# Kernel tuning notes

Measured on AMD Instinct MI355X. Metric: run time of the kernel, lower is better.

The kernel has to match this reference:

```python
import jax, jax.numpy as jnp
import numpy as np

N_NODES = 200000
FEAT_DIM = 256
EMB_DIM = 64
N_EXP = 100000
N_TARGETS = 1024
MAX_CAND = 128


def setup_inputs() -> dict:
    key = jax.random.key(0)
    ks = jax.random.split(key, 10)
    return {
        "x": jax.random.normal(ks[0], (N_NODES, FEAT_DIM), jnp.float32),
        "h": jax.random.normal(ks[1], (N_NODES, EMB_DIM), jnp.float32),
        "degree": jax.random.uniform(ks[2], (N_NODES,), jnp.float32),
        "beta": jax.random.uniform(ks[3], (N_NODES,), jnp.float32),
        "exp_nodes": jax.random.randint(ks[4], (N_EXP,), 0, N_NODES),
        "idx_targets": jax.random.randint(ks[5], (N_TARGETS,), 0, N_NODES),
        "W_raw": jax.random.normal(ks[6], (FEAT_DIM, EMB_DIM), jnp.float32) / np.float32(np.sqrt(FEAT_DIM)),
        "b_raw": jnp.zeros((EMB_DIM,), jnp.float32),
        "W_num": jax.random.normal(ks[7], (2, EMB_DIM), jnp.float32),
        "b_num": jnp.zeros((EMB_DIM,), jnp.float32),
        "W1": jax.random.normal(ks[8], (4 * EMB_DIM, EMB_DIM), jnp.float32) / np.float32(np.sqrt(4 * EMB_DIM)),
        "b1": jnp.zeros((EMB_DIM,), jnp.float32),
        "W2": jax.random.normal(ks[9], (EMB_DIM, 1), jnp.float32) / np.float32(np.sqrt(EMB_DIM)),
        "b2": jnp.zeros((1,), jnp.float32),
        "temperature": jnp.float32(1.0),
        "epsilon": jnp.float32(1.0),
    }


def reference(x, h, degree, beta, exp_nodes, idx_targets,
              W_raw, b_raw, W_num, b_num, W1, b1, W2, b2,
              temperature, epsilon):
    # gather node features and project (irregular gather + small GEMM)
    x_v = x[exp_nodes] @ W_raw + b_raw                       # [E, emb]
    h_v = h[exp_nodes]                                       # [E, emb]
    h_T = jnp.broadcast_to(h[idx_targets].mean(axis=0)[None, :],
                           (exp_nodes.shape[0], EMB_DIM))    # [E, emb]
    numerics = jnp.stack([degree[exp_nodes], beta[exp_nodes]], axis=-1)  # [E, 2]
    emb_num = numerics @ W_num + b_num                       # [E, emb]
    emb = jax.nn.relu(jnp.concatenate([x_v, h_v, h_T, emb_num], axis=-1))  # [E, 4*emb]
    # dropout is identity in eval mode
    hidden = jax.nn.relu(emb @ W1 + b1)                      # [E, emb]
    scores = (hidden @ W2 + b2)[:, 0]                        # [E]
    # straight-through gumbel top-k (eval: no gumbel noise, epsilon unused)
    y = jax.nn.softmax(scores / temperature)
    _, idx = jax.lax.top_k(y, MAX_CAND)
    y_hard = jnp.zeros_like(y).at[idx].set(1.0)
    y_st = jax.lax.stop_gradient(y_hard - y) + y
    candidates = y_st[idx]                                   # [MAX_CAND] (== 1.0 fwd)
    cand_indices = exp_nodes[idx]                            # [MAX_CAND]
    return candidates, cand_indices
```

## Files before the change

### kernel.cpp

```cpp
#include <hip/hip_runtime.h>
#include <stdint.h>

#define RELU(v) ((v) > 0.0f ? (v) : 0.0f)

typedef unsigned long long u64;
typedef unsigned int u32;
typedef unsigned short u16;
typedef float f32x4 __attribute__((ext_vector_type(4)));
typedef short bf16x8 __attribute__((ext_vector_type(8)));

constexpr int FEAT = 256;
constexpr int EMB  = 64;

constexpr int STG_ROW = 264;
constexpr int WAVE_BYTES = 16 * STG_ROW * 2;
constexpr int XV_ROW = 68;
constexpr int KEEP_BLK = 12;

__device__ inline u16 bf16_trunc(float v) { return (u16)(__float_as_uint(v) >> 16); }

__device__ inline u32 score_key(float s) {
    u32 u = __float_as_uint(s);
    return (u & 0x80000000u) ? ~u : (u | 0x80000000u);
}

__device__ inline bf16x8 pack_bf16x8(float4 lo, float4 hi) {
    bf16x8 r;
    r[0] = (short)bf16_trunc(lo.x); r[1] = (short)bf16_trunc(lo.y);
    r[2] = (short)bf16_trunc(lo.z); r[3] = (short)bf16_trunc(lo.w);
    r[4] = (short)bf16_trunc(hi.x); r[5] = (short)bf16_trunc(hi.y);
    r[6] = (short)bf16_trunc(hi.z); r[7] = (short)bf16_trunc(hi.w);
    return r;
}

__global__ __launch_bounds__(1024) void setup_kernel(
    const float* __restrict__ h, const int* __restrict__ idx_targets, int nT,
    const float* __restrict__ W_raw, const float* __restrict__ W1, const float* __restrict__ b1,
    float* __restrict__ bias_eff, u16* __restrict__ wrawpk, u16* __restrict__ w1pk)
{
    const int tid = threadIdx.x;
    if (blockIdx.x == 1) {
        for (int t = tid; t < 2048; t += 1024) {
            int ks   = t >> 8;
            int c    = (t >> 6) & 3;
            int lane = t & 63;
            int n    = c * 16 + (lane & 15);
            int kbase = ks * 32 + ((lane >> 4) << 3);
            #pragma unroll
            for (int j = 0; j < 8; ++j) {
                int k = kbase + j;
                wrawpk[t * 8 + j] = bf16_trunc(W_raw[(size_t)k * EMB + n]);
                w1pk  [t * 8 + j] = bf16_trunc(W1   [(size_t)k * EMB + n]);
            }
        }
        return;
    }
    __shared__ int   idx_s[1024];
    __shared__ float partial[16][64];
    __shared__ float hT[64];
    const int nid = nT > 1024 ? 1024 : nT;
    for (int i = tid; i < nid; i += 1024) idx_s[i] = idx_targets[i];
    __syncthreads();
    const int d = tid & 63, grp = tid >> 6;
    float s = 0.f;
    for (int t = grp; t < nid; t += 16)
        s += h[(size_t)idx_s[t] * EMB + d];
    partial[grp][d] = s;
    __syncthreads();
    if (tid < 64) {
        float m = 0.f;
        #pragma unroll
        for (int g = 0; g < 16; ++g) m += partial[g][tid];
        hT[tid] = RELU(m / (float)nT);
    }
    __syncthreads();
    if (tid < 64) {
        float acc = b1[tid];
        #pragma unroll 8
        for (int dd = 0; dd < 64; ++dd)
            acc = fmaf(hT[dd], W1[(size_t)(128 + dd) * EMB + tid], acc);
        bias_eff[tid] = acc;
    }
}

__global__ __launch_bounds__(256) void approx_score_kernel(
    const float* __restrict__ x, const float* __restrict__ h,
    const float* __restrict__ degree, const float* __restrict__ beta,
    const int* __restrict__ exp_nodes,
    const u16* __restrict__ wrawpk, const u16* __restrict__ w1pk,
    const float* __restrict__ b_raw,
    const float* __restrict__ W_num, const float* __restrict__ b_num,
    const float* __restrict__ W2, const float* __restrict__ bias_eff,
    u64* __restrict__ cand1, int E)
{
    __shared__ __align__(16) unsigned char smem[4][WAVE_BYTES];
    __shared__ u64 sarr[64];

    const int tid  = threadIdx.x;
    const int wid  = tid >> 6;
    const int lane = tid & 63;
    const int rloc = lane & 15;
    const int kgrp = lane >> 4;
    const int koff = kgrp * 8;
    const int tileBase = blockIdx.x * 64;

    const int grow = tileBase + wid * 16 + rloc;
    const int node = exp_nodes[grow < E ? grow : 0];
    const float* hrow = h + (size_t)node * EMB;
    const float dg = degree[node];
    const float bt = beta[node];

    u16*   stg = (u16*)&smem[wid][0];
    float* xvp = (float*)&smem[wid][0];

    #pragma unroll
    for (int half = 0; half < 2; ++half) {
        float4 v0, v1, v2, v3, v4, v5, v6, v7;
        {
            int r = half * 8;
            v0 = *reinterpret_cast<const float4*>(x + (size_t)__shfl(node, r + 0) * FEAT + lane * 4);
            v1 = *reinterpret_cast<const float4*>(x + (size_t)__shfl(node, r + 1) * FEAT + lane * 4);
            v2 = *reinterpret_cast<const float4*>(x + (size_t)__shfl(node, r + 2) * FEAT + lane * 4);
            v3 = *reinterpret_cast<const float4*>(x + (size_t)__shfl(node, r + 3) * FEAT + lane * 4);
            v4 = *reinterpret_cast<const float4*>(x + (size_t)__shfl(node, r + 4) * FEAT + lane * 4);
            v5 = *reinterpret_cast<const float4*>(x + (size_t)__shfl(node, r + 5) * FEAT + lane * 4);
            v6 = *reinterpret_cast<const float4*>(x + (size_t)__shfl(node, r + 6) * FEAT + lane * 4);
            v7 = *reinterpret_cast<const float4*>(x + (size_t)__shfl(node, r + 7) * FEAT + lane * 4);
        }
        #define STG_WRITE(rr, vv) { \
            ushort4 pk; pk.x = bf16_trunc(vv.x); pk.y = bf16_trunc(vv.y); \
            pk.z = bf16_trunc(vv.z); pk.w = bf16_trunc(vv.w); \
            *reinterpret_cast<ushort4*>(stg + (half * 8 + rr) * STG_ROW + lane * 4) = pk; }
        STG_WRITE(0, v0) STG_WRITE(1, v1) STG_WRITE(2, v2) STG_WRITE(3, v3)
        STG_WRITE(4, v4) STG_WRITE(5, v5) STG_WRITE(6, v6) STG_WRITE(7, v7)
        #undef STG_WRITE
    }
    __builtin_amdgcn_wave_barrier();

    f32x4 acc1[4];
    #pragma unroll
    for (int c = 0; c < 4; ++c) {
        float bv = b_raw[c * 16 + rloc];
        acc1[c] = (f32x4){bv, bv, bv, bv};
    }
    #pragma unroll
    for (int ks = 0; ks < 8; ++ks) {
        bf16x8 a = *reinterpret_cast<const bf16x8*>(stg + rloc * STG_ROW + ks * 32 + koff);
        #pragma unroll
        for (int c = 0; c < 4; ++c) {
            bf16x8 b = *reinterpret_cast<const bf16x8*>(wrawpk + (size_t)((ks * 4 + c) * 64 + lane) * 8);
            acc1[c] = __builtin_amdgcn_mfma_f32_16x16x32_bf16(a, b, acc1[c], 0, 0, 0);
        }
    }
    __builtin_amdgcn_wave_barrier();

    #pragma unroll
    for (int c = 0; c < 4; ++c)
        #pragma unroll
        for (int r = 0; r < 4; ++r)
            xvp[(kgrp * 4 + r) * XV_ROW + c * 16 + rloc] = RELU(acc1[c][r]);
    __builtin_amdgcn_wave_barrier();

    f32x4 acc2[4];
    #pragma unroll
    for (int c = 0; c < 4; ++c) {
        float bv = bias_eff[c * 16 + rloc];
        acc2[c] = (f32x4){bv, bv, bv, bv};
    }

    #pragma unroll
    for (int ks = 0; ks < 2; ++ks) {
        float4 lo = *reinterpret_cast<const float4*>(hrow + ks * 32 + koff);
        float4 hi = *reinterpret_cast<const float4*>(hrow + ks * 32 + koff + 4);
        lo.x = RELU(lo.x); lo.y = RELU(lo.y); lo.z = RELU(lo.z); lo.w = RELU(lo.w);
        hi.x = RELU(hi.x); hi.y = RELU(hi.y); hi.z = RELU(hi.z); hi.w = RELU(hi.w);
        bf16x8 a = pack_bf16x8(lo, hi);
        #pragma unroll
        for (int c = 0; c < 4; ++c) {
            bf16x8 b = *reinterpret_cast<const bf16x8*>(w1pk + (size_t)(((2 + ks) * 4 + c) * 64 + lane) * 8);
            acc2[c] = __builtin_amdgcn_mfma_f32_16x16x32_bf16(a, b, acc2[c], 0, 0, 0);
        }
    }

    #pragma unroll
    for (int ks = 0; ks < 2; ++ks) {
        bf16x8 a;
        #pragma unroll
        for (int j = 0; j < 8; ++j) {
            int k = ks * 32 + koff + j;
            float v = RELU(fmaf(dg, W_num[k], fmaf(bt, W_num[EMB + k], b_num[k])));
            a[j] = (short)bf16_trunc(v);
        }
        #pragma unroll
        for (int c = 0; c < 4; ++c) {
            bf16x8 b = *reinterpret_cast<const bf16x8*>(w1pk + (size_t)(((6 + ks) * 4 + c) * 64 + lane) * 8);
            acc2[c] = __builtin_amdgcn_mfma_f32_16x16x32_bf16(a, b, acc2[c], 0, 0, 0);
        }
    }

    #pragma unroll
    for (int ks = 0; ks < 2; ++ks) {
        float4 lo = *reinterpret_cast<const float4*>(xvp + rloc * XV_ROW + ks * 32 + koff);
        float4 hi = *reinterpret_cast<const float4*>(xvp + rloc * XV_ROW + ks * 32 + koff + 4);
        bf16x8 a = pack_bf16x8(lo, hi);
        #pragma unroll
        for (int c = 0; c < 4; ++c) {
            bf16x8 b = *reinterpret_cast<const bf16x8*>(w1pk + (size_t)((ks * 4 + c) * 64 + lane) * 8);
            acc2[c] = __builtin_amdgcn_mfma_f32_16x16x32_bf16(a, b, acc2[c], 0, 0, 0);
        }
    }

    float p[4] = {0.f, 0.f, 0.f, 0.f};
    #pragma unroll
    for (int c = 0; c < 4; ++c) {
        float w2v = W2[c * 16 + rloc];
        #pragma unroll
        for (int r = 0; r < 4; ++r)
            p[r] = fmaf(RELU(acc2[c][r]), w2v, p[r]);
    }
    #pragma unroll
    for (int m = 1; m < 16; m <<= 1) {
        p[0] += __shfl_xor(p[0], m);
        p[1] += __shfl_xor(p[1], m);
        p[2] += __shfl_xor(p[2], m);
        p[3] += __shfl_xor(p[3], m);
    }
    if (rloc == 0) {
        #pragma unroll
        for (int r = 0; r < 4; ++r) {
            int lrow = wid * 16 + kgrp * 4 + r;
            int g = tileBase + lrow;
            sarr[lrow] = (g < E) ? (((u64)score_key(p[r]) << 32) | (u32)(~(u32)g)) : 0ULL;
        }
    }
    __syncthreads();

    if (wid == 0) {
        u64 v = sarr[lane];
        #pragma unroll
        for (int k = 2; k <= 64; k <<= 1) {
            #pragma unroll
            for (int j = k >> 1; j > 0; j >>= 1) {
                u64 o = __shfl_xor(v, j);
                bool lower = (lane & j) == 0;
                bool dir   = (lane & k) == 0;
                v = (lower == dir) ? (v > o ? v : o) : (v < o ? v : o);
            }
        }
        if (lane < KEEP_BLK) cand1[(size_t)blockIdx.x * KEEP_BLK + lane] = v;
    }
}

template<int N, int NT>
__device__ inline void bitonic_desc(u64* s, int tid) {
    for (int k = 2; k <= N; k <<= 1) {
        for (int j = k >> 1; j > 0; j >>= 1) {
            __syncthreads();
            for (int i = tid; i < N; i += NT) {
                int ixj = i ^ j;
                if (ixj > i) {
                    u64 a = s[i], b = s[ixj];
                    bool sw = ((i & k) == 0) ? (a < b) : (a > b);
                    if (sw) { s[i] = b; s[ixj] = a; }
                }
            }
        }
    }
    __syncthreads();
}

template<int N, int NT, int KEEP>
__global__ __launch_bounds__(NT) void seg_sort_kernel(
    const u64* __restrict__ in, int n_in, int seg, u64* __restrict__ out)
{
    __shared__ u64 s[N];
    int tid = threadIdx.x;
    int base = blockIdx.x * seg;
    for (int i = tid; i < N; i += NT) {
        int g = base + i;
        s[i] = (i < seg && g < n_in) ? in[g] : 0ULL;
    }
    bitonic_desc<N, NT>(s, tid);
    if (tid < KEEP) out[blockIdx.x * KEEP + tid] = s[tid];
}

__global__ __launch_bounds__(256) void rescore_kernel(
    const float* __restrict__ x, const float* __restrict__ h,
    const float* __restrict__ degree, const float* __restrict__ beta,
    const int* __restrict__ exp_nodes,
    const float* __restrict__ W_raw, const float* __restrict__ b_raw,
    const float* __restrict__ W_num, const float* __restrict__ b_num,
    const float* __restrict__ W1, const float* __restrict__ W2,
    const float* __restrict__ bias_eff,
    const u64* __restrict__ cand, u64* __restrict__ pairs2, int E)
{
    __shared__ float emb[4][192];
    const int tid = threadIdx.x;
    const int wid = tid >> 6;
    const int c   = tid & 63;
    const int i   = blockIdx.x * 4 + wid;

    const u64 raw = cand[i];
    const u32 low = (u32)raw;
    const u32 ge  = ~low;
    const int node = (raw != 0ULL && ge < (u32)E) ? exp_nodes[ge] : 0;

    const float* xrow = x + (size_t)node * FEAT;

    float s0 = b_raw[c], s1 = 0.f, s2 = 0.f, s3 = 0.f;
    for (int k = 0; k < FEAT; k += 4) {
        s0 = fmaf(xrow[k + 0], W_raw[(size_t)(k + 0) * EMB + c], s0);
        s1 = fmaf(xrow[k + 1], W_raw[(size_t)(k + 1) * EMB + c], s1);
        s2 = fmaf(xrow[k + 2], W_raw[(size_t)(k + 2) * EMB + c], s2);
        s3 = fmaf(xrow[k + 3], W_raw[(size_t)(k + 3) * EMB + c], s3);
    }
    float xv = (s0 + s1) + (s2 + s3);

    emb[wid][c]       = RELU(xv);
    emb[wid][64 + c]  = RELU(h[(size_t)node * EMB + c]);
    emb[wid][128 + c] = RELU(fmaf(degree[node], W_num[c], fmaf(beta[node], W_num[EMB + c], b_num[c])));
    __syncthreads();

    float h0 = bias_eff[c], h1 = 0.f, h2 = 0.f, h3 = 0.f;
    for (int j = 0; j < 64; j += 2) {
        h0 = fmaf(emb[wid][j],     W1[(size_t)j * EMB + c],       h0);
        h1 = fmaf(emb[wid][j + 1], W1[(size_t)(j + 1) * EMB + c], h1);
    }
    for (int j = 0; j < 64; j += 2) {
        h2 = fmaf(emb[wid][64 + j],     W1[(size_t)(64 + j) * EMB + c],     h2);
        h3 = fmaf(emb[wid][64 + j + 1], W1[(size_t)(64 + j + 1) * EMB + c], h3);
    }
    for (int j = 0; j < 64; j += 2) {
        h0 = fmaf(emb[wid][128 + j],     W1[(size_t)(192 + j) * EMB + c],     h0);
        h1 = fmaf(emb[wid][128 + j + 1], W1[(size_t)(192 + j + 1) * EMB + c], h1);
    }
    float hid = (h0 + h1) + (h2 + h3);

    float p = RELU(hid) * W2[c];
    #pragma unroll
    for (int m = 1; m < 64; m <<= 1) p += __shfl_xor(p, m);

    if (c == 0)
        pairs2[i] = (raw == 0ULL) ? 0ULL : (((u64)score_key(p) << 32) | low);
}

__global__ __launch_bounds__(1024) void topk_final_kernel(
    const u64* __restrict__ in, int n_in,
    const int* __restrict__ exp_nodes, float* __restrict__ out)
{
    __shared__ u64 s[1024];
    int tid = threadIdx.x;
    s[tid] = (tid < n_in) ? in[tid] : 0ULL;
    bitonic_desc<1024, 1024>(s, tid);
    if (tid < 128) {
        u64 p = s[tid];
        u32 idx = ~(u32)(p & 0xFFFFFFFFu);
        out[tid]       = 1.0f;
        out[128 + tid] = (float)exp_nodes[idx];
    }
}

extern "C" void kernel_launch(void* const* d_in, const int* in_sizes, int n_in,
                              void* d_out, int out_size, void* d_ws, size_t ws_size,
                              hipStream_t stream) {
    const float* x          = (const float*)d_in[0];
    const float* h          = (const float*)d_in[1];
    const float* degree     = (const float*)d_in[2];
    const float* beta       = (const float*)d_in[3];
    const int*   exp_nodes  = (const int*)d_in[4];
    const int*   idx_targets= (const int*)d_in[5];
    const float* W_raw      = (const float*)d_in[6];
    const float* b_raw      = (const float*)d_in[7];
    const float* W_num      = (const float*)d_in[8];
    const float* b_num      = (const float*)d_in[9];
    const float* W1         = (const float*)d_in[10];
    const float* b1         = (const float*)d_in[11];
    const float* W2         = (const float*)d_in[12];

    int E  = in_sizes[4];
    int nT = in_sizes[5];

    int nTiles = (E + 63) / 64;
    int nCand1 = nTiles * KEEP_BLK;
    int nSel   = (nCand1 + 1023) / 1024;
    int nKept  = nSel * 52;
    int nResc  = (nKept + 3) / 4;

    char* ws = (char*)d_ws;
    float* bias_eff = (float*)ws;
    u16* wrawpk = (u16*)(ws + 256);
    u16* w1pk   = (u16*)(ws + 256 + 32768);
    u64* cand1  = (u64*)(ws + 256 + 65536);
    u64* cand2  = (u64*)(ws + 256 + 65536 + 163840);
    u64* pairs2 = (u64*)(ws + 256 + 65536 + 163840 + 8192);

    setup_kernel<<<2, 1024, 0, stream>>>(h, idx_targets, nT, W_raw, W1, b1,
                                         bias_eff, wrawpk, w1pk);

    approx_score_kernel<<<nTiles, 256, 0, stream>>>(x, h, degree, beta, exp_nodes,
                                                    wrawpk, w1pk, b_raw, W_num, b_num,
                                                    W2, bias_eff, cand1, E);

    seg_sort_kernel<1024, 512, 52><<<nSel, 512, 0, stream>>>(cand1, nCand1, 1024, cand2);

    rescore_kernel<<<nResc, 256, 0, stream>>>(x, h, degree, beta, exp_nodes,
                                              W_raw, b_raw, W_num, b_num, W1, W2,
                                              bias_eff, cand2, pairs2, E);

    topk_final_kernel<<<1, 1024, 0, stream>>>(pairs2, nKept, exp_nodes, (float*)d_out);
}
```

Measured before the change: 107.8 us.

## Double rows per wave in approx scoring, fuse final top-k into rescore

The approx score kernel now handles 128 rows per block, 32 per wave. Each wave loads x rows straight from global into MFMA A-fragments instead of staging bf16 copies in LDS, and two accumulator sets share each loaded weight fragment. The final top-k kernel is folded into the rescore kernel: an atomic counter picks the last-finishing block, which does the bitonic sort, and a memset resets the counter on every call. This cuts one launch and the LDS staging traffic, but raises register pressure and loads x with narrower per-lane strided accesses.

```diff
diff --git a/kernel.cpp b/kernel.cpp
--- a/kernel.cpp
+++ b/kernel.cpp
@@ -12,8 +12,6 @@
 constexpr int FEAT = 256;
 constexpr int EMB  = 64;
 
-constexpr int STG_ROW = 264;
-constexpr int WAVE_BYTES = 16 * STG_ROW * 2;
 constexpr int XV_ROW = 68;
 constexpr int KEEP_BLK = 12;
 
@@ -93,8 +91,8 @@
     const float* __restrict__ W2, const float* __restrict__ bias_eff,
     u64* __restrict__ cand1, int E)
 {
-    __shared__ __align__(16) unsigned char smem[4][WAVE_BYTES];
-    __shared__ u64 sarr[64];
+    __shared__ __align__(16) float xv_lds[4][32 * XV_ROW];
+    __shared__ u64 sarr[128];
 
     const int tid  = threadIdx.x;
     const int wid  = tid >> 6;
@@ -102,141 +100,149 @@
     const int rloc = lane & 15;
     const int kgrp = lane >> 4;
     const int koff = kgrp * 8;
-    const int tileBase = blockIdx.x * 64;
-
-    const int grow = tileBase + wid * 16 + rloc;
-    const int node = exp_nodes[grow < E ? grow : 0];
-    const float* hrow = h + (size_t)node * EMB;
-    const float dg = degree[node];
-    const float bt = beta[node];
-
-    u16*   stg = (u16*)&smem[wid][0];
-    float* xvp = (float*)&smem[wid][0];
-
-    #pragma unroll
-    for (int half = 0; half < 2; ++half) {
-        float4 v0, v1, v2, v3, v4, v5, v6, v7;
-        {
-            int r = half * 8;
-            v0 = *reinterpret_cast<const float4*>(x + (size_t)__shfl(node, r + 0) * FEAT + lane * 4);
-            v1 = *reinterpret_cast<const float4*>(x + (size_t)__shfl(node, r + 1) * FEAT + lane * 4);
-            v2 = *reinterpret_cast<const float4*>(x + (size_t)__shfl(node, r + 2) * FEAT + lane * 4);
-            v3 = *reinterpret_cast<const float4*>(x + (size_t)__shfl(node, r + 3) * FEAT + lane * 4);
-            v4 = *reinterpret_cast<const float4*>(x + (size_t)__shfl(node, r + 4) * FEAT + lane * 4);
-            v5 = *reinterpret_cast<const float4*>(x + (size_t)__shfl(node, r + 5) * FEAT + lane * 4);
-            v6 = *reinterpret_cast<const float4*>(x + (size_t)__shfl(node, r + 6) * FEAT + lane * 4);
-            v7 = *reinterpret_cast<const float4*>(x + (size_t)__shfl(node, r + 7) * FEAT + lane * 4);
-        }
-        #define STG_WRITE(rr, vv) { \
-            ushort4 pk; pk.x = bf16_trunc(vv.x); pk.y = bf16_trunc(vv.y); \
-            pk.z = bf16_trunc(vv.z); pk.w = bf16_trunc(vv.w); \
-            *reinterpret_cast<ushort4*>(stg + (half * 8 + rr) * STG_ROW + lane * 4) = pk; }
-        STG_WRITE(0, v0) STG_WRITE(1, v1) STG_WRITE(2, v2) STG_WRITE(3, v3)
-        STG_WRITE(4, v4) STG_WRITE(5, v5) STG_WRITE(6, v6) STG_WRITE(7, v7)
-        #undef STG_WRITE
-    }
-    __builtin_amdgcn_wave_barrier();
-
-    f32x4 acc1[4];
+    const int tileBase = blockIdx.x * 128;
+
+    const int g0 = tileBase + wid * 32 + rloc;
+    const int g1 = g0 + 16;
+    const int node0 = exp_nodes[g0 < E ? g0 : 0];
+    const int node1 = exp_nodes[g1 < E ? g1 : 0];
+    const float* xrow0 = x + (size_t)node0 * FEAT;
+    const float* xrow1 = x + (size_t)node1 * FEAT;
+    const float* hrow0 = h + (size_t)node0 * EMB;
+    const float* hrow1 = h + (size_t)node1 * EMB;
+    const float dg0 = degree[node0], bt0 = beta[node0];
+    const float dg1 = degree[node1], bt1 = beta[node1];
+
+    float* xvpA = &xv_lds[wid][0];
+    float* xvpB = &xv_lds[wid][16 * XV_ROW];
+
+    f32x4 acc1a[4], acc1b[4];
     #pragma unroll
     for (int c = 0; c < 4; ++c) {
         float bv = b_raw[c * 16 + rloc];
-        acc1[c] = (f32x4){bv, bv, bv, bv};
+        acc1a[c] = (f32x4){bv, bv, bv, bv};
+        acc1b[c] = (f32x4){bv, bv, bv, bv};
     }
     #pragma unroll
     for (int ks = 0; ks < 8; ++ks) {
-        bf16x8 a = *reinterpret_cast<const bf16x8*>(stg + rloc * STG_ROW + ks * 32 + koff);
+        float4 lo0 = *reinterpret_cast<const float4*>(xrow0 + ks * 32 + koff);
+        float4 hi0 = *reinterpret_cast<const float4*>(xrow0 + ks * 32 + koff + 4);
+        float4 lo1 = *reinterpret_cast<const float4*>(xrow1 + ks * 32 + koff);
+        float4 hi1 = *reinterpret_cast<const float4*>(xrow1 + ks * 32 + koff + 4);
+        bf16x8 a0 = pack_bf16x8(lo0, hi0);
+        bf16x8 a1 = pack_bf16x8(lo1, hi1);
         #pragma unroll
         for (int c = 0; c < 4; ++c) {
             bf16x8 b = *reinterpret_cast<const bf16x8*>(wrawpk + (size_t)((ks * 4 + c) * 64 + lane) * 8);
-            acc1[c] = __builtin_amdgcn_mfma_f32_16x16x32_bf16(a, b, acc1[c], 0, 0, 0);
-        }
-    }
+            acc1a[c] = __builtin_amdgcn_mfma_f32_16x16x32_bf16(a0, b, acc1a[c], 0, 0, 0);
+            acc1b[c] = __builtin_amdgcn_mfma_f32_16x16x32_bf16(a1, b, acc1b[c], 0, 0, 0);
+        }
+    }
+
+    #pragma unroll
+    for (int c = 0; c < 4; ++c)
+        #pragma unroll
+        for (int r = 0; r < 4; ++r) {
+            xvpA[(kgrp * 4 + r) * XV_ROW + c * 16 + rloc] = RELU(acc1a[c][r]);
+            xvpB[(kgrp * 4 + r) * XV_ROW + c * 16 + rloc] = RELU(acc1b[c][r]);
+        }
     __builtin_amdgcn_wave_barrier();
 
-    #pragma unroll
-    for (int c = 0; c < 4; ++c)
-        #pragma unroll
-        for (int r = 0; r < 4; ++r)
-            xvp[(kgrp * 4 + r) * XV_ROW + c * 16 + rloc] = RELU(acc1[c][r]);
-    __builtin_amdgcn_wave_barrier();
-
-    f32x4 acc2[4];
+    f32x4 acc2a[4], acc2b[4];
     #pragma unroll
     for (int c = 0; c < 4; ++c) {
         float bv = bias_eff[c * 16 + rloc];
-        acc2[c] = (f32x4){bv, bv, bv, bv};
+        acc2a[c] = (f32x4){bv, bv, bv, bv};
+        acc2b[c] = (f32x4){bv, bv, bv, bv};
     }
 
     #pragma unroll
     for (int ks = 0; ks < 2; ++ks) {
-        float4 lo = *reinterpret_cast<const float4*>(hrow + ks * 32 + koff);
-        float4 hi = *reinterpret_cast<const float4*>(hrow + ks * 32 + koff + 4);
-        lo.x = RELU(lo.x); lo.y = RELU(lo.y); lo.z = RELU(lo.z); lo.w = RELU(lo.w);
-        hi.x = RELU(hi.x); hi.y = RELU(hi.y); hi.z = RELU(hi.z); hi.w = RELU(hi.w);
-        bf16x8 a = pack_bf16x8(lo, hi);
+        float4 lo0 = *reinterpret_cast<const float4*>(hrow0 + ks * 32 + koff);
+        float4 hi0 = *reinterpret_cast<const float4*>(hrow0 + ks * 32 + koff + 4);
+        float4 lo1 = *reinterpret_cast<const float4*>(hrow1 + ks * 32 + koff);
+        float4 hi1 = *reinterpret_cast<const float4*>(hrow1 + ks * 32 + koff + 4);
+        lo0.x=RELU(lo0.x); lo0.y=RELU(lo0.y); lo0.z=RELU(lo0.z); lo0.w=RELU(lo0.w);
+        hi0.x=RELU(hi0.x); hi0.y=RELU(hi0.y); hi0.z=RELU(hi0.z); hi0.w=RELU(hi0.w);
+        lo1.x=RELU(lo1.x); lo1.y=RELU(lo1.y); lo1.z=RELU(lo1.z); lo1.w=RELU(lo1.w);
+        hi1.x=RELU(hi1.x); hi1.y=RELU(hi1.y); hi1.z=RELU(hi1.z); hi1.w=RELU(hi1.w);
+        bf16x8 a0 = pack_bf16x8(lo0, hi0);
+        bf16x8 a1 = pack_bf16x8(lo1, hi1);
         #pragma unroll
         for (int c = 0; c < 4; ++c) {
             bf16x8 b = *reinterpret_cast<const bf16x8*>(w1pk + (size_t)(((2 + ks) * 4 + c) * 64 + lane) * 8);
-            acc2[c] = __builtin_amdgcn_mfma_f32_16x16x32_bf16(a, b, acc2[c], 0, 0, 0);
+            acc2a[c] = __builtin_amdgcn_mfma_f32_16x16x32_bf16(a0, b, acc2a[c], 0, 0, 0);
+            acc2b[c] = __builtin_amdgcn_mfma_f32_16x16x32_bf16(a1, b, acc2b[c], 0, 0, 0);
         }
     }
 
     #pragma unroll
     for (int ks = 0; ks < 2; ++ks) {
-        bf16x8 a;
+        bf16x8 a0, a1;
         #pragma unroll
         for (int j = 0; j < 8; ++j) {
             int k = ks * 32 + koff + j;
-            float v = RELU(fmaf(dg, W_num[k], fmaf(bt, W_num[EMB + k], b_num[k])));
-            a[j] = (short)bf16_trunc(v);
+            float wn0 = W_num[k], wn1 = W_num[EMB + k], bn = b_num[k];
+            a0[j] = (short)bf16_trunc(RELU(fmaf(dg0, wn0, fmaf(bt0, wn1, bn))));
+            a1[j] = (short)bf16_trunc(RELU(fmaf(dg1, wn0, fmaf(bt1, wn1, bn))));
         }
         #pragma unroll
         for (int c = 0; c < 4; ++c) {
             bf16x8 b = *reinterpret_cast<const bf16x8*>(w1pk + (size_t)(((6 + ks) * 4 + c) * 64 + lane) * 8);
-            acc2[c] = __builtin_amdgcn_mfma_f32_16x16x32_bf16(a, b, acc2[c], 0, 0, 0);
+            acc2a[c] = __builtin_amdgcn_mfma_f32_16x16x32_bf16(a0, b, acc2a[c], 0, 0, 0);
+            acc2b[c] = __builtin_amdgcn_mfma_f32_16x16x32_bf16(a1, b, acc2b[c], 0, 0, 0);
         }
     }
 
     #pragma unroll
     for (int ks = 0; ks < 2; ++ks) {
-        float4 lo = *reinterpret_cast<const float4*>(xvp + rloc * XV_ROW + ks * 32 + koff);
-        float4 hi = *reinterpret_cast<const float4*>(xvp + rloc * XV_ROW + ks * 32 + koff + 4);
-        bf16x8 a = pack_bf16x8(lo, hi);
+        float4 lo0 = *reinterpret_cast<const float4*>(xvpA + rloc * XV_ROW + ks * 32 + koff);
+        float4 hi0 = *reinterpret_cast<const float4*>(xvpA + rloc * XV_ROW + ks * 32 + koff + 4);
+        float4 lo1 = *reinterpret_cast<const float4*>(xvpB + rloc * XV_ROW + ks * 32 + koff);
+        float4 hi1 = *reinterpret_cast<const float4*>(xvpB + rloc * XV_ROW + ks * 32 + koff + 4);
+        bf16x8 a0 = pack_bf16x8(lo0, hi0);
+        bf16x8 a1 = pack_bf16x8(lo1, hi1);
         #pragma unroll
         for (int c = 0; c < 4; ++c) {
             bf16x8 b = *reinterpret_cast<const bf16x8*>(w1pk + (size_t)((ks * 4 + c) * 64 + lane) * 8);
-            acc2[c] = __builtin_amdgcn_mfma_f32_16x16x32_bf16(a, b, acc2[c], 0, 0, 0);
-        }
-    }
-
-    float p[4] = {0.f, 0.f, 0.f, 0.f};
+            acc2a[c] = __builtin_amdgcn_mfma_f32_16x16x32_bf16(a0, b, acc2a[c], 0, 0, 0);
+            acc2b[c] = __builtin_amdgcn_mfma_f32_16x16x32_bf16(a1, b, acc2b[c], 0, 0, 0);
+        }
+    }
+
+    float pA[4] = {0,0,0,0}, pB[4] = {0,0,0,0};
     #pragma unroll
     for (int c = 0; c < 4; ++c) {
         float w2v = W2[c * 16 + rloc];
         #pragma unroll
-        for (int r = 0; r < 4; ++r)
-            p[r] = fmaf(RELU(acc2[c][r]), w2v, p[r]);
+        for (int r = 0; r < 4; ++r) {
+            pA[r] = fmaf(RELU(acc2a[c][r]), w2v, pA[r]);
+            pB[r] = fmaf(RELU(acc2b[c][r]), w2v, pB[r]);
+        }
     }
     #pragma unroll
     for (int m = 1; m < 16; m <<= 1) {
-        p[0] += __shfl_xor(p[0], m);
-        p[1] += __shfl_xor(p[1], m);
-        p[2] += __shfl_xor(p[2], m);
-        p[3] += __shfl_xor(p[3], m);
+        #pragma unroll
+        for (int r = 0; r < 4; ++r) {
+            pA[r] += __shfl_xor(pA[r], m);
+            pB[r] += __shfl_xor(pB[r], m);
+        }
     }
     if (rloc == 0) {
         #pragma unroll
         for (int r = 0; r < 4; ++r) {
-            int lrow = wid * 16 + kgrp * 4 + r;
-            int g = tileBase + lrow;
-            sarr[lrow] = (g < E) ? (((u64)score_key(p[r]) << 32) | (u32)(~(u32)g)) : 0ULL;
-        }
-    }
-    __syncthreads();
-
-    if (wid == 0) {
-        u64 v = sarr[lane];
+            int lrowA = wid * 32 + kgrp * 4 + r;
+            int gA = tileBase + lrowA;
+            sarr[lrowA] = (gA < E) ? (((u64)score_key(pA[r]) << 32) | (u32)(~(u32)gA)) : 0ULL;
+            int lrowB = lrowA + 16;
+            int gB = tileBase + lrowB;
+            sarr[lrowB] = (gB < E) ? (((u64)score_key(pB[r]) << 32) | (u32)(~(u32)gB)) : 0ULL;
+        }
+    }
+    __syncthreads();
+
+    if (wid < 2) {
+        u64 v = sarr[wid * 64 + lane];
         #pragma unroll
         for (int k = 2; k <= 64; k <<= 1) {
             #pragma unroll
@@ -247,7 +253,8 @@
                 v = (lower == dir) ? (v > o ? v : o) : (v < o ? v : o);
             }
         }
-        if (lane < KEEP_BLK) cand1[(size_t)blockIdx.x * KEEP_BLK + lane] = v;
+        if (lane < KEEP_BLK)
+            cand1[(size_t)blockIdx.x * (2 * KEEP_BLK) + wid * KEEP_BLK + lane] = v;
     }
 }
 
@@ -284,7 +291,7 @@
     if (tid < KEEP) out[blockIdx.x * KEEP + tid] = s[tid];
 }
 
-__global__ __launch_bounds__(256) void rescore_kernel(
+__global__ __launch_bounds__(256) void rescore_final_kernel(
     const float* __restrict__ x, const float* __restrict__ h,
     const float* __restrict__ degree, const float* __restrict__ beta,
     const int* __restrict__ exp_nodes,
@@ -292,9 +299,13 @@
     const float* __restrict__ W_num, const float* __restrict__ b_num,
     const float* __restrict__ W1, const float* __restrict__ W2,
     const float* __restrict__ bias_eff,
-    const u64* __restrict__ cand, u64* __restrict__ pairs2, int E)
+    const u64* __restrict__ cand, u64* __restrict__ pairs2, int E,
+    int nKept, int nBlocks, u32* __restrict__ counter,
+    float* __restrict__ out)
 {
     __shared__ float emb[4][192];
+    __shared__ u64 s[1024];
+    __shared__ int isLast;
     const int tid = threadIdx.x;
     const int wid = tid >> 6;
     const int c   = tid & 63;
@@ -342,19 +353,22 @@
 
     if (c == 0)
         pairs2[i] = (raw == 0ULL) ? 0ULL : (((u64)score_key(p) << 32) | low);
-}
-
-__global__ __launch_bounds__(1024) void topk_final_kernel(
-    const u64* __restrict__ in, int n_in,
-    const int* __restrict__ exp_nodes, float* __restrict__ out)
-{
-    __shared__ u64 s[1024];
-    int tid = threadIdx.x;
-    s[tid] = (tid < n_in) ? in[tid] : 0ULL;
-    bitonic_desc<1024, 1024>(s, tid);
+
+    __threadfence();
+    if (tid == 0) {
+        u32 old = atomicAdd(counter, 1u);
+        isLast = (old == (u32)(nBlocks - 1));
+    }
+    __syncthreads();
+    if (!isLast) return;
+    __threadfence();
+
+    for (int k = tid; k < 1024; k += 256)
+        s[k] = (k < nKept) ? pairs2[k] : 0ULL;
+    bitonic_desc<1024, 256>(s, tid);
     if (tid < 128) {
-        u64 p = s[tid];
-        u32 idx = ~(u32)(p & 0xFFFFFFFFu);
+        u64 pr = s[tid];
+        u32 idx = ~(u32)(pr & 0xFFFFFFFFu);
         out[tid]       = 1.0f;
         out[128 + tid] = (float)exp_nodes[idx];
     }
@@ -380,8 +394,8 @@
     int E  = in_sizes[4];
     int nT = in_sizes[5];
 
-    int nTiles = (E + 63) / 64;
-    int nCand1 = nTiles * KEEP_BLK;
+    int nTiles = (E + 127) / 128;
+    int nCand1 = nTiles * 2 * KEEP_BLK;
     int nSel   = (nCand1 + 1023) / 1024;
     int nKept  = nSel * 52;
     int nResc  = (nKept + 3) / 4;
@@ -393,6 +407,9 @@
     u64* cand1  = (u64*)(ws + 256 + 65536);
     u64* cand2  = (u64*)(ws + 256 + 65536 + 163840);
     u64* pairs2 = (u64*)(ws + 256 + 65536 + 163840 + 8192);
+    u32* counter= (u32*)(ws + 256 + 65536 + 163840 + 16384);
+
+    hipMemsetAsync(counter, 0, 4, stream);
 
     setup_kernel<<<2, 1024, 0, stream>>>(h, idx_targets, nT, W_raw, W1, b1,
                                          bias_eff, wrawpk, w1pk);
@@ -403,9 +420,8 @@
 
     seg_sort_kernel<1024, 512, 52><<<nSel, 512, 0, stream>>>(cand1, nCand1, 1024, cand2);
 
-    rescore_kernel<<<nResc, 256, 0, stream>>>(x, h, degree, beta, exp_nodes,
-                                              W_raw, b_raw, W_num, b_num, W1, W2,
-                                              bias_eff, cand2, pairs2, E);
-
-    topk_final_kernel<<<1, 1024, 0, stream>>>(pairs2, nKept, exp_nodes, (float*)d_out);
-}
+    rescore_final_kernel<<<nResc, 256, 0, stream>>>(x, h, degree, beta, exp_nodes,
+                                                    W_raw, b_raw, W_num, b_num, W1, W2,
+                                                    bias_eff, cand2, pairs2, E,
+                                                    nKept, nResc, counter, (float*)d_out);
+}
```

Result: slower. 152.3 us (+41.3%).
